# Kernel tuning notes

Hardware: AMD Instinct MI355X
Metric: run time of the kernel (lower is better)

## Reference

```python
import jax, jax.numpy as jnp
import numpy as np

N = 100000   # nodes
E = 1000000  # edges
IN, HID, OUT = 128, 64, 64


def setup_inputs() -> dict:
    key = jax.random.key(0)
    ks = jax.random.split(key, 6)
    x = jax.random.normal(ks[0], (N, IN), dtype=jnp.float32)
    edge_index = jax.random.randint(ks[1], (2, E), 0, N, dtype=jnp.int64)
    edge_attr = jax.random.uniform(ks[2], (E,), dtype=jnp.float32)
    # Glorot-style init like PyG GCNConv (weight [in, out], bias zeros)
    W1 = jax.random.normal(ks[3], (IN, HID), dtype=jnp.float32) * (1.0 / np.sqrt(IN))
    b1 = jnp.zeros((HID,), dtype=jnp.float32)
    W2 = jax.random.normal(ks[4], (HID, OUT), dtype=jnp.float32) * (1.0 / np.sqrt(HID))
    b2 = jnp.zeros((OUT,), dtype=jnp.float32)
    return {"x": x, "edge_index": edge_index, "edge_attr": edge_attr,
            "W1": W1, "b1": b1, "W2": W2, "b2": b2}


def gcn_conv(x, edge_index, edge_weight, W, b):
    """GCNConv: add self-loops, symmetric normalization, linear + scatter-add."""
    n = x.shape[0]
    row, col = edge_index[0], edge_index[1]
    loop = jnp.arange(n, dtype=row.dtype)
    row = jnp.concatenate([row, loop])
    col = jnp.concatenate([col, loop])
    w = jnp.concatenate([edge_weight, jnp.ones((n,), dtype=x.dtype)])
    deg = jax.ops.segment_sum(w, col, num_segments=n)              # [N]
    dinv = jnp.where(deg > 0, jax.lax.rsqrt(deg), 0.0)
    norm = dinv[row] * w * dinv[col]                               # [E+N]
    h = x @ W                                                      # [N, out]
    agg = jax.ops.segment_sum(h[row] * norm[:, None], col, num_segments=n)
    return agg + b


def reference(x, edge_index, edge_attr, W1, b1, W2, b2):
    h = jax.nn.relu(gcn_conv(x, edge_index, edge_attr, W1, b1))
    return jax.nn.relu(gcn_conv(h, edge_index, edge_attr, W2, b2))
```

## Files before the change

### kernel.cpp

```cpp
#include <hip/hip_runtime.h>


#define BNODES 128
#define LB 7
#define MAXBKT 1024
#define EPT 16
#define EPB (256 * EPT)

typedef __attribute__((ext_vector_type(8))) short bf16x8;
typedef __attribute__((ext_vector_type(4))) float f32x4;

__device__ __forceinline__ unsigned short f2bf(float f) {
    unsigned u = __float_as_uint(f);
    u = (u + 0x7FFF + ((u >> 16) & 1)) >> 16;
    return (unsigned short)u;
}
__device__ __forceinline__ float bf2f(unsigned short h) {
    return __uint_as_float(((unsigned)h) << 16);
}

__device__ __forceinline__ int waveIncScan(int v, int lane) {
    #pragma unroll
    for (int d = 1; d < 64; d <<= 1) {
        int u = __shfl_up(v, d, 64);
        if (lane >= d) v += u;
    }
    return v;
}

__device__ __forceinline__ int blockIncScan(int v, int t, int* wt) {
    int lane = t & 63, w = t >> 6;
    int s = waveIncScan(v, lane);
    if (lane == 63) wt[w] = s;
    __syncthreads();
    int add = 0;
    #pragma unroll
    for (int i = 0; i < 3; ++i) if (i < w) add += wt[i];
    return s + add;
}


__global__ __launch_bounds__(256) void hist_kernel(
    const int* __restrict__ col, int* __restrict__ H, int E, int NBKT,
    const float* __restrict__ W1, const float* __restrict__ W2,
    unsigned short* __restrict__ WT1, unsigned short* __restrict__ WT2, int NEB)
{
    int t = threadIdx.x, blk = blockIdx.x;
    if (blk >= NEB) {
        int i = (blk - NEB) * 256 + t;
        if (i < 64 * 128) {
            int c = i >> 7, k = i & 127;
            WT1[i] = f2bf(W1[k * 64 + c]);
        } else if (i < 64 * 128 + 64 * 64) {
            int j = i - 64 * 128;
            int c = j >> 6, k = j & 63;
            WT2[j] = f2bf(W2[k * 64 + c]);
        }
        return;
    }
    __shared__ int h[MAXBKT];
    for (int b = t; b < NBKT; b += 256) h[b] = 0;
    __syncthreads();
    int base = blk * EPB;
    #pragma unroll
    for (int i = 0; i < EPT; ++i) {
        int e = base + i * 256 + t;
        if (e < E) atomicAdd(&h[col[e] >> LB], 1);
    }
    __syncthreads();
    for (int b = t; b < NBKT; b += 256) H[blk * NBKT + b] = h[b];
}

__global__ __launch_bounds__(256) void rowscan_kernel(
    int* __restrict__ H, int* __restrict__ rowSum, int NEB, int NBKT)
{
    __shared__ int wt[4];
    int b = blockIdx.x, t = threadIdx.x;
    int v = (t < NEB) ? H[t * NBKT + b] : 0;
    int incl = blockIncScan(v, t, wt);
    if (t < NEB) H[t * NBKT + b] = incl - v;
    if (t == 255) rowSum[b] = incl;
}

__global__ __launch_bounds__(256) void bktscan_kernel(
    const int* __restrict__ rowSum, int* __restrict__ bktStart, int NBKT)
{
    __shared__ int wt[4];
    int t = threadIdx.x;
    int v[4]; int sum = 0;
    #pragma unroll
    for (int k = 0; k < 4; ++k) {
        int i = t * 4 + k;
        v[k] = (i < NBKT) ? rowSum[i] : 0;
        sum += v[k];
    }
    int incl = blockIncScan(sum, t, wt);
    int excl = incl - sum;
    #pragma unroll
    for (int k = 0; k < 4; ++k) {
        int i = t * 4 + k;
        if (i < NBKT) bktStart[i] = excl;
        excl += v[k];
    }
    if (t == 255) bktStart[NBKT] = incl;
}

__global__ __launch_bounds__(256) void scatter_kernel(
    const int* __restrict__ row, const int* __restrict__ col,
    const float* __restrict__ w, const int* __restrict__ H,
    const int* __restrict__ bktStart, int2* __restrict__ sedge1, int E, int NBKT)
{
    __shared__ int cur[MAXBKT];
    int t = threadIdx.x, blk = blockIdx.x;
    for (int b = t; b < NBKT; b += 256) cur[b] = bktStart[b] + H[blk * NBKT + b];
    __syncthreads();
    int base = blk * EPB;
    #pragma unroll
    for (int i = 0; i < EPT; ++i) {
        int e = base + i * 256 + t;
        if (e < E) {
            int c = col[e];
            int b = c >> LB;
            int pos = atomicAdd(&cur[b], 1);
            int2 pk;
            pk.x = row[e] | ((c & (BNODES - 1)) << 20);
            pk.y = __float_as_int(w[e]);
            sedge1[pos] = pk;
        }
    }
}

__global__ __launch_bounds__(256) void fine_kernel(
    const int2* __restrict__ sedge1, const int* __restrict__ bktStart,
    int2* __restrict__ sedge2, int* __restrict__ nodeStart,
    int* __restrict__ nodeCnt, float* __restrict__ dinv, int n)
{
    __shared__ int cnt[BNODES];
    __shared__ float wsum[BNODES];
    __shared__ int off[BNODES];
    __shared__ int cur[BNODES];
    __shared__ int wt[4];
    int b = blockIdx.x, t = threadIdx.x;
    if (t < BNODES) { cnt[t] = 0; wsum[t] = 1.0f; }
    __syncthreads();
    int s = bktStart[b], e = bktStart[b + 1];
    for (int j = s + t; j < e; j += 256) {
        int2 pk = sedge1[j];
        int ld = pk.x >> 20;
        atomicAdd(&cnt[ld], 1);
        atomicAdd(&wsum[ld], __int_as_float(pk.y));
    }
    __syncthreads();
    int v = (t < BNODES) ? cnt[t] : 0;
    int incl = blockIncScan(v, t, wt);
    if (t < BNODES) { off[t] = s + incl - v; cur[t] = s + incl - v; }
    __syncthreads();
    int node = b * BNODES + t;
    if (t < BNODES && node < n) {
        nodeStart[node] = off[t];
        nodeCnt[node] = cnt[t];
        dinv[node] = rsqrtf(wsum[t]);
    }
    for (int j = s + t; j < e; j += 256) {
        int2 pk = sedge1[j];
        int ld = pk.x >> 20;
        int pos = atomicAdd(&cur[ld], 1);
        sedge2[pos] = make_int2(pk.x & 0xFFFFF, pk.y);
    }
}

template<int K, bool IN_BF16>
__global__ __launch_bounds__(256) void gemm_mfma_kernel(
    const void* __restrict__ Xv, const unsigned short* __restrict__ WT,
    const float* __restrict__ dinv, unsigned short* __restrict__ G, int n)
{
    constexpr int ROWB = 2 * K;
    constexpr int SLOTS = K / 8;
    __shared__ char smem[64 * ROWB * 2];
    char* xs = smem;
    char* ws = smem + 64 * ROWB;
    const int tid = threadIdx.x;
    const int nodeBase = blockIdx.x * 64;

    for (int q = tid; q < 64 * SLOTS; q += 256) {
        int r = q / SLOTS, s = q % SLOTS;
        uint4 v = *(const uint4*)(WT + r * K + s * 8);
        *(uint4*)(ws + r * ROWB + ((s ^ (r & 7)) * 16)) = v;
    }
    constexpr int CPR = K / 4;
    if constexpr (IN_BF16) {
        const unsigned short* X = (const unsigned short*)Xv;
        for (int q = tid; q < 64 * CPR; q += 256) {
            int r = q / CPR, c = q % CPR;
            int node = nodeBase + r;
            uint2 v = make_uint2(0u, 0u);
            if (node < n) v = *(const uint2*)(X + (size_t)node * K + c * 4);
            *(uint2*)(xs + r * ROWB + (((c >> 1) ^ (r & 7)) * 16) + (c & 1) * 8) = v;
        }
    } else {
        const float* X = (const float*)Xv;
        for (int q = tid; q < 64 * CPR; q += 256) {
            int r = q / CPR, c = q % CPR;
            int node = nodeBase + r;
            float4 v = make_float4(0.f, 0.f, 0.f, 0.f);
            if (node < n) v = *(const float4*)(X + (size_t)node * K + c * 4);
            ushort4 h;
            h.x = f2bf(v.x); h.y = f2bf(v.y); h.z = f2bf(v.z); h.w = f2bf(v.w);
            *(ushort4*)(xs + r * ROWB + (((c >> 1) ^ (r & 7)) * 16) + (c & 1) * 8) = h;
        }
    }
    __syncthreads();

    const int lane = tid & 63;
    const int w = tid >> 6;
    const int lr = lane & 15;
    const int lk = lane >> 4;
    const int arow = (w << 4) + lr;

    f32x4 acc[4] = {};
    #pragma unroll
    for (int kb = 0; kb < K / 32; ++kb) {
        int s = kb * 4 + lk;
        bf16x8 a = *(bf16x8*)(xs + arow * ROWB + ((s ^ (arow & 7)) * 16));
        #pragma unroll
        for (int cb = 0; cb < 4; ++cb) {
            int c = cb * 16 + lr;
            bf16x8 b = *(bf16x8*)(ws + c * ROWB + ((s ^ (c & 7)) * 16));
            acc[cb] = __builtin_amdgcn_mfma_f32_16x16x32_bf16(a, b, acc[cb], 0, 0, 0);
        }
    }

    int rowbase = nodeBase + (w << 4) + (lk << 2);
    #pragma unroll
    for (int j = 0; j < 4; ++j) {
        int node = rowbase + j;
        if (node >= n) continue;
        float dv = dinv[node];
        #pragma unroll
        for (int cb = 0; cb < 4; ++cb)
            G[(size_t)node * 64 + cb * 16 + lr] = f2bf(acc[cb][j] * dv);
    }
}

__global__ __launch_bounds__(256) void aggmm_kernel(
    const unsigned short* __restrict__ G1, const int2* __restrict__ sedge2,
    const int* __restrict__ nodeStart, const int* __restrict__ nodeCnt,
    const float* __restrict__ dinv, const float* __restrict__ bias,
    const unsigned short* __restrict__ WT2, unsigned short* __restrict__ G2, int n)
{
    constexpr int ROWB = 128;
    __shared__ char smem[64 * ROWB * 2];
    char* xs = smem;
    char* ws = smem + 64 * ROWB;
    const int tid = threadIdx.x;
    const int nodeBase = blockIdx.x * 64;

    for (int q = tid; q < 64 * 8; q += 256) {
        int r = q >> 3, s = q & 7;
        uint4 v = *(const uint4*)(WT2 + r * 64 + s * 8);
        *(uint4*)(ws + r * ROWB + ((s ^ (r & 7)) * 16)) = v;
    }

    int p = tid & 15;
    float4 bb = *(const float4*)&bias[p * 4];
    #pragma unroll
    for (int pass = 0; pass < 4; ++pass) {
        int r = pass * 16 + (tid >> 4);
        int node = nodeBase + r;
        float4 o = make_float4(0.f, 0.f, 0.f, 0.f);
        if (node < n) {
            ushort4 sv = *(const ushort4*)&G1[(size_t)node * 64 + p * 4];
            float4 a0 = make_float4(bf2f(sv.x), bf2f(sv.y), bf2f(sv.z), bf2f(sv.w));
            float4 a1 = make_float4(0.f, 0.f, 0.f, 0.f);
            int s = nodeStart[node];
            int e_end = s + nodeCnt[node];
            int j = s;
            for (; j + 1 < e_end; j += 2) {
                int2 pk0 = sedge2[j];
                int2 pk1 = sedge2[j + 1];
                float w0 = __int_as_float(pk0.y);
                float w1 = __int_as_float(pk1.y);
                ushort4 g0 = *(const ushort4*)&G1[(size_t)pk0.x * 64 + p * 4];
                ushort4 g1 = *(const ushort4*)&G1[(size_t)pk1.x * 64 + p * 4];
                a0.x = fmaf(w0, bf2f(g0.x), a0.x); a0.y = fmaf(w0, bf2f(g0.y), a0.y);
                a0.z = fmaf(w0, bf2f(g0.z), a0.z); a0.w = fmaf(w0, bf2f(g0.w), a0.w);
                a1.x = fmaf(w1, bf2f(g1.x), a1.x); a1.y = fmaf(w1, bf2f(g1.y), a1.y);
                a1.z = fmaf(w1, bf2f(g1.z), a1.z); a1.w = fmaf(w1, bf2f(g1.w), a1.w);
            }
            if (j < e_end) {
                int2 pk = sedge2[j];
                float w = __int_as_float(pk.y);
                ushort4 g = *(const ushort4*)&G1[(size_t)pk.x * 64 + p * 4];
                a0.x = fmaf(w, bf2f(g.x), a0.x); a0.y = fmaf(w, bf2f(g.y), a0.y);
                a0.z = fmaf(w, bf2f(g.z), a0.z); a0.w = fmaf(w, bf2f(g.w), a0.w);
            }
            float di = dinv[node];
            o.x = fmaxf(fmaf(di, a0.x + a1.x, bb.x), 0.f);
            o.y = fmaxf(fmaf(di, a0.y + a1.y, bb.y), 0.f);
            o.z = fmaxf(fmaf(di, a0.z + a1.z, bb.z), 0.f);
            o.w = fmaxf(fmaf(di, a0.w + a1.w, bb.w), 0.f);
        }
        ushort4 h;
        h.x = f2bf(o.x); h.y = f2bf(o.y); h.z = f2bf(o.z); h.w = f2bf(o.w);
        *(ushort4*)(xs + r * ROWB + (((p >> 1) ^ (r & 7)) * 16) + (p & 1) * 8) = h;
    }
    __syncthreads();

    const int lane = tid & 63;
    const int w = tid >> 6;
    const int lr = lane & 15;
    const int lk = lane >> 4;
    const int arow = (w << 4) + lr;

    f32x4 acc[4] = {};
    #pragma unroll
    for (int kb = 0; kb < 2; ++kb) {
        int s = kb * 4 + lk;
        bf16x8 a = *(bf16x8*)(xs + arow * ROWB + ((s ^ (arow & 7)) * 16));
        #pragma unroll
        for (int cb = 0; cb < 4; ++cb) {
            int c = cb * 16 + lr;
            bf16x8 b = *(bf16x8*)(ws + c * ROWB + ((s ^ (c & 7)) * 16));
            acc[cb] = __builtin_amdgcn_mfma_f32_16x16x32_bf16(a, b, acc[cb], 0, 0, 0);
        }
    }

    int rowbase = nodeBase + (w << 4) + (lk << 2);
    #pragma unroll
    for (int j = 0; j < 4; ++j) {
        int node = rowbase + j;
        if (node >= n) continue;
        float dv = dinv[node];
        #pragma unroll
        for (int cb = 0; cb < 4; ++cb)
            G2[(size_t)node * 64 + cb * 16 + lr] = f2bf(acc[cb][j] * dv);
    }
}

__global__ __launch_bounds__(256) void agg_kernel(
    const unsigned short* __restrict__ G, const int2* __restrict__ sedge2,
    const int* __restrict__ nodeStart, const int* __restrict__ nodeCnt,
    const float* __restrict__ dinv, const float* __restrict__ bias,
    float* __restrict__ OUT, int n)
{
    int t = blockIdx.x * blockDim.x + threadIdx.x;
    if (t >= n * 16) return;
    int node = t >> 4, p = t & 15;

    ushort4 sv = *(const ushort4*)&G[(size_t)node * 64 + p * 4];
    float4 a0 = make_float4(bf2f(sv.x), bf2f(sv.y), bf2f(sv.z), bf2f(sv.w));
    float4 a1 = make_float4(0.f, 0.f, 0.f, 0.f);

    int s = nodeStart[node];
    int e_end = s + nodeCnt[node];
    int j = s;
    for (; j + 1 < e_end; j += 2) {
        int2 pk0 = sedge2[j];
        int2 pk1 = sedge2[j + 1];
        float w0 = __int_as_float(pk0.y);
        float w1 = __int_as_float(pk1.y);
        ushort4 g0 = *(const ushort4*)&G[(size_t)pk0.x * 64 + p * 4];
        ushort4 g1 = *(const ushort4*)&G[(size_t)pk1.x * 64 + p * 4];
        a0.x = fmaf(w0, bf2f(g0.x), a0.x); a0.y = fmaf(w0, bf2f(g0.y), a0.y);
        a0.z = fmaf(w0, bf2f(g0.z), a0.z); a0.w = fmaf(w0, bf2f(g0.w), a0.w);
        a1.x = fmaf(w1, bf2f(g1.x), a1.x); a1.y = fmaf(w1, bf2f(g1.y), a1.y);
        a1.z = fmaf(w1, bf2f(g1.z), a1.z); a1.w = fmaf(w1, bf2f(g1.w), a1.w);
    }
    if (j < e_end) {
        int2 pk = sedge2[j];
        float w = __int_as_float(pk.y);
        ushort4 g = *(const ushort4*)&G[(size_t)pk.x * 64 + p * 4];
        a0.x = fmaf(w, bf2f(g.x), a0.x); a0.y = fmaf(w, bf2f(g.y), a0.y);
        a0.z = fmaf(w, bf2f(g.z), a0.z); a0.w = fmaf(w, bf2f(g.w), a0.w);
    }

    float di = dinv[node];
    float4 bb = *(const float4*)&bias[p * 4];
    float4 o;
    o.x = fmaxf(fmaf(di, a0.x + a1.x, bb.x), 0.f);
    o.y = fmaxf(fmaf(di, a0.y + a1.y, bb.y), 0.f);
    o.z = fmaxf(fmaf(di, a0.z + a1.z, bb.z), 0.f);
    o.w = fmaxf(fmaf(di, a0.w + a1.w, bb.w), 0.f);
    *(float4*)&OUT[(size_t)node * 64 + p * 4] = o;
}

extern "C" void kernel_launch(void* const* d_in, const int* in_sizes, int n_in,
                              void* d_out, int out_size, void* d_ws, size_t ws_size,
                              hipStream_t stream) {
    const float* x     = (const float*)d_in[0];
    const int*   eidx  = (const int*)d_in[1];
    const float* eattr = (const float*)d_in[2];
    const float* W1    = (const float*)d_in[3];
    const float* b1    = (const float*)d_in[4];
    const float* W2    = (const float*)d_in[5];
    const float* b2    = (const float*)d_in[6];
    float* out = (float*)d_out;

    const int n = in_sizes[0] / 128;
    const int E = in_sizes[2];
    const int* row = eidx;
    const int* col = eidx + E;

    const int NBKT = (n + BNODES - 1) / BNODES;
    const int NEB  = (E + EPB - 1) / EPB;

    int2*  sedge1 = (int2*)d_ws;
    int2*  sedge2 = sedge1 + (size_t)E;
    unsigned short* g1 = (unsigned short*)(sedge2 + (size_t)E);
    unsigned short* g2 = g1 + (size_t)n * 64;
    unsigned short* WT1 = g2 + (size_t)n * 64;
    unsigned short* WT2 = WT1 + 64 * 128;
    float* dinv      = (float*)(WT2 + 64 * 64);
    int*   nodeStart = (int*)(dinv + n);
    int*   nodeCnt   = nodeStart + n;
    int*   H         = nodeCnt + n;
    int*   rowSum    = H + (size_t)NEB * NBKT;
    int*   bktStart  = rowSum + NBKT;

    const int nbG = (n + 63) / 64;
    const int nbA = (int)(((size_t)n * 16 + 255) / 256);

    hist_kernel<<<NEB + 48, 256, 0, stream>>>(col, H, E, NBKT, W1, W2, WT1, WT2, NEB);
    rowscan_kernel<<<NBKT, 256, 0, stream>>>(H, rowSum, NEB, NBKT);
    bktscan_kernel<<<1, 256, 0, stream>>>(rowSum, bktStart, NBKT);
    scatter_kernel<<<NEB, 256, 0, stream>>>(row, col, eattr, H, bktStart, sedge1, E, NBKT);
    fine_kernel<<<NBKT, 256, 0, stream>>>(sedge1, bktStart, sedge2, nodeStart, nodeCnt, dinv, n);

    gemm_mfma_kernel<128, false><<<nbG, 256, 0, stream>>>(x, WT1, dinv, g1, n);
    aggmm_kernel<<<nbG, 256, 0, stream>>>(g1, sedge2, nodeStart, nodeCnt, dinv, b1, WT2, g2, n);
    agg_kernel<<<nbA, 256, 0, stream>>>(g2, sedge2, nodeStart, nodeCnt, dinv, b2, out, n);
}
```

Measured before the change: 129.1 us.

## Merge edge scatter with first GEMM and apply dinv scaling in fine kernel

The first-layer GEMM no longer needs dinv, so it is launched as extra blocks of the scatter kernel and runs alongside the edge bucketing. The dinv row scaling of g1 moves into fine_kernel as a read-modify-write pass over each bucket's nodes. The gather loops are also unrolled by four with separate accumulators to give more memory-level parallelism. The trade-offs are an extra read and write of g1, a second bf16 rounding step, and a larger shared-memory footprint for the scatter blocks.

Measured after the change: 133.6 us. 3.5% more time.

```diff
diff --git a/kernel.cpp b/kernel.cpp
--- a/kernel.cpp
+++ b/kernel.cpp
@@ -105,121 +105,69 @@
     if (t == 255) bktStart[NBKT] = incl;
 }
 
-__global__ __launch_bounds__(256) void scatter_kernel(
+__global__ __launch_bounds__(256) void scatter_gemm_kernel(
     const int* __restrict__ row, const int* __restrict__ col,
     const float* __restrict__ w, const int* __restrict__ H,
-    const int* __restrict__ bktStart, int2* __restrict__ sedge1, int E, int NBKT)
-{
-    __shared__ int cur[MAXBKT];
-    int t = threadIdx.x, blk = blockIdx.x;
-    for (int b = t; b < NBKT; b += 256) cur[b] = bktStart[b] + H[blk * NBKT + b];
-    __syncthreads();
-    int base = blk * EPB;
-    #pragma unroll
-    for (int i = 0; i < EPT; ++i) {
-        int e = base + i * 256 + t;
-        if (e < E) {
-            int c = col[e];
-            int b = c >> LB;
-            int pos = atomicAdd(&cur[b], 1);
-            int2 pk;
-            pk.x = row[e] | ((c & (BNODES - 1)) << 20);
-            pk.y = __float_as_int(w[e]);
-            sedge1[pos] = pk;
+    const int* __restrict__ bktStart, int2* __restrict__ sedge1,
+    int E, int NBKT, int NEB,
+    const float* __restrict__ X, const unsigned short* __restrict__ WT,
+    unsigned short* __restrict__ G, int n)
+{
+    __shared__ char smem[64 * 256 * 2];
+    const int t = threadIdx.x;
+    const int blk = blockIdx.x;
+
+    if (blk < NEB) {
+        int* cur = (int*)smem;
+        for (int b = t; b < NBKT; b += 256) cur[b] = bktStart[b] + H[blk * NBKT + b];
+        __syncthreads();
+        int base = blk * EPB;
+        #pragma unroll
+        for (int i = 0; i < EPT; ++i) {
+            int e = base + i * 256 + t;
+            if (e < E) {
+                int c = col[e];
+                int b = c >> LB;
+                int pos = atomicAdd(&cur[b], 1);
+                int2 pk;
+                pk.x = row[e] | ((c & (BNODES - 1)) << 20);
+                pk.y = __float_as_int(w[e]);
+                sedge1[pos] = pk;
+            }
         }
-    }
-}
-
-__global__ __launch_bounds__(256) void fine_kernel(
-    const int2* __restrict__ sedge1, const int* __restrict__ bktStart,
-    int2* __restrict__ sedge2, int* __restrict__ nodeStart,
-    int* __restrict__ nodeCnt, float* __restrict__ dinv, int n)
-{
-    __shared__ int cnt[BNODES];
-    __shared__ float wsum[BNODES];
-    __shared__ int off[BNODES];
-    __shared__ int cur[BNODES];
-    __shared__ int wt[4];
-    int b = blockIdx.x, t = threadIdx.x;
-    if (t < BNODES) { cnt[t] = 0; wsum[t] = 1.0f; }
-    __syncthreads();
-    int s = bktStart[b], e = bktStart[b + 1];
-    for (int j = s + t; j < e; j += 256) {
-        int2 pk = sedge1[j];
-        int ld = pk.x >> 20;
-        atomicAdd(&cnt[ld], 1);
-        atomicAdd(&wsum[ld], __int_as_float(pk.y));
-    }
-    __syncthreads();
-    int v = (t < BNODES) ? cnt[t] : 0;
-    int incl = blockIncScan(v, t, wt);
-    if (t < BNODES) { off[t] = s + incl - v; cur[t] = s + incl - v; }
-    __syncthreads();
-    int node = b * BNODES + t;
-    if (t < BNODES && node < n) {
-        nodeStart[node] = off[t];
-        nodeCnt[node] = cnt[t];
-        dinv[node] = rsqrtf(wsum[t]);
-    }
-    for (int j = s + t; j < e; j += 256) {
-        int2 pk = sedge1[j];
-        int ld = pk.x >> 20;
-        int pos = atomicAdd(&cur[ld], 1);
-        sedge2[pos] = make_int2(pk.x & 0xFFFFF, pk.y);
-    }
-}
-
-template<int K, bool IN_BF16>
-__global__ __launch_bounds__(256) void gemm_mfma_kernel(
-    const void* __restrict__ Xv, const unsigned short* __restrict__ WT,
-    const float* __restrict__ dinv, unsigned short* __restrict__ G, int n)
-{
-    constexpr int ROWB = 2 * K;
-    constexpr int SLOTS = K / 8;
-    __shared__ char smem[64 * ROWB * 2];
+        return;
+    }
+
+    constexpr int K = 128, ROWB = 256, SLOTS = 16, CPR = 32;
     char* xs = smem;
     char* ws = smem + 64 * ROWB;
-    const int tid = threadIdx.x;
-    const int nodeBase = blockIdx.x * 64;
-
-    for (int q = tid; q < 64 * SLOTS; q += 256) {
+    const int nodeBase = (blk - NEB) * 64;
+
+    for (int q = t; q < 64 * SLOTS; q += 256) {
         int r = q / SLOTS, s = q % SLOTS;
         uint4 v = *(const uint4*)(WT + r * K + s * 8);
         *(uint4*)(ws + r * ROWB + ((s ^ (r & 7)) * 16)) = v;
     }
-    constexpr int CPR = K / 4;
-    if constexpr (IN_BF16) {
-        const unsigned short* X = (const unsigned short*)Xv;
-        for (int q = tid; q < 64 * CPR; q += 256) {
-            int r = q / CPR, c = q % CPR;
-            int node = nodeBase + r;
-            uint2 v = make_uint2(0u, 0u);
-            if (node < n) v = *(const uint2*)(X + (size_t)node * K + c * 4);
-            *(uint2*)(xs + r * ROWB + (((c >> 1) ^ (r & 7)) * 16) + (c & 1) * 8) = v;
-        }
-    } else {
-        const float* X = (const float*)Xv;
-        for (int q = tid; q < 64 * CPR; q += 256) {
-            int r = q / CPR, c = q % CPR;
-            int node = nodeBase + r;
-            float4 v = make_float4(0.f, 0.f, 0.f, 0.f);
-            if (node < n) v = *(const float4*)(X + (size_t)node * K + c * 4);
-            ushort4 h;
-            h.x = f2bf(v.x); h.y = f2bf(v.y); h.z = f2bf(v.z); h.w = f2bf(v.w);
-            *(ushort4*)(xs + r * ROWB + (((c >> 1) ^ (r & 7)) * 16) + (c & 1) * 8) = h;
-        }
-    }
-    __syncthreads();
-
-    const int lane = tid & 63;
-    const int w = tid >> 6;
+    for (int q = t; q < 64 * CPR; q += 256) {
+        int r = q / CPR, c = q % CPR;
+        int node = nodeBase + r;
+        float4 v = make_float4(0.f, 0.f, 0.f, 0.f);
+        if (node < n) v = *(const float4*)(X + (size_t)node * K + c * 4);
+        ushort4 h;
+        h.x = f2bf(v.x); h.y = f2bf(v.y); h.z = f2bf(v.z); h.w = f2bf(v.w);
+        *(ushort4*)(xs + r * ROWB + (((c >> 1) ^ (r & 7)) * 16) + (c & 1) * 8) = h;
+    }
+    __syncthreads();
+
+    const int lane = t & 63;
+    const int wv = t >> 6;
     const int lr = lane & 15;
     const int lk = lane >> 4;
-    const int arow = (w << 4) + lr;
+    const int arow = (wv << 4) + lr;
 
     f32x4 acc[4] = {};
     #pragma unroll
-    for (int kb = 0; kb < K / 32; ++kb) {
+    for (int kb = 0; kb < 4; ++kb) {
         int s = kb * 4 + lk;
         bf16x8 a = *(bf16x8*)(xs + arow * ROWB + ((s ^ (arow & 7)) * 16));
         #pragma unroll
@@ -230,16 +178,114 @@
         }
     }
 
-    int rowbase = nodeBase + (w << 4) + (lk << 2);
+    int rowbase = nodeBase + (wv << 4) + (lk << 2);
     #pragma unroll
     for (int j = 0; j < 4; ++j) {
         int node = rowbase + j;
         if (node >= n) continue;
-        float dv = dinv[node];
         #pragma unroll
         for (int cb = 0; cb < 4; ++cb)
-            G[(size_t)node * 64 + cb * 16 + lr] = f2bf(acc[cb][j] * dv);
-    }
+            G[(size_t)node * 64 + cb * 16 + lr] = f2bf(acc[cb][j]);
+    }
+}
+
+__global__ __launch_bounds__(256) void fine_kernel(
+    const int2* __restrict__ sedge1, const int* __restrict__ bktStart,
+    int2* __restrict__ sedge2, int* __restrict__ nodeStart,
+    int* __restrict__ nodeCnt, float* __restrict__ dinv,
+    unsigned short* __restrict__ g1, int n)
+{
+    __shared__ int cnt[BNODES];
+    __shared__ float wsum[BNODES];
+    __shared__ int off[BNODES];
+    __shared__ int cur[BNODES];
+    __shared__ float dloc[BNODES];
+    __shared__ int wt[4];
+    int b = blockIdx.x, t = threadIdx.x;
+    if (t < BNODES) { cnt[t] = 0; wsum[t] = 1.0f; }
+    __syncthreads();
+    int s = bktStart[b], e = bktStart[b + 1];
+    for (int j = s + t; j < e; j += 256) {
+        int2 pk = sedge1[j];
+        int ld = pk.x >> 20;
+        atomicAdd(&cnt[ld], 1);
+        atomicAdd(&wsum[ld], __int_as_float(pk.y));
+    }
+    __syncthreads();
+    int v = (t < BNODES) ? cnt[t] : 0;
+    int incl = blockIncScan(v, t, wt);
+    if (t < BNODES) {
+        off[t] = s + incl - v;
+        cur[t] = s + incl - v;
+        dloc[t] = rsqrtf(wsum[t]);
+    }
+    __syncthreads();
+    int node = b * BNODES + t;
+    if (t < BNODES && node < n) {
+        nodeStart[node] = off[t];
+        nodeCnt[node] = cnt[t];
+        dinv[node] = dloc[t];
+    }
+    for (int j = s + t; j < e; j += 256) {
+        int2 pk = sedge1[j];
+        int ld = pk.x >> 20;
+        int pos = atomicAdd(&cur[ld], 1);
+        sedge2[pos] = make_int2(pk.x & 0xFFFFF, pk.y);
+    }
+    for (int q = t; q < BNODES * 8; q += 256) {
+        int r = q >> 3, cc = q & 7;
+        int nd = b * BNODES + r;
+        if (nd >= n) continue;
+        float dv = dloc[r];
+        size_t offb = (size_t)nd * 64 + cc * 8;
+        ushort4 u0 = *(const ushort4*)(g1 + offb);
+        ushort4 u1 = *(const ushort4*)(g1 + offb + 4);
+        u0.x = f2bf(bf2f(u0.x) * dv); u0.y = f2bf(bf2f(u0.y) * dv);
+        u0.z = f2bf(bf2f(u0.z) * dv); u0.w = f2bf(bf2f(u0.w) * dv);
+        u1.x = f2bf(bf2f(u1.x) * dv); u1.y = f2bf(bf2f(u1.y) * dv);
+        u1.z = f2bf(bf2f(u1.z) * dv); u1.w = f2bf(bf2f(u1.w) * dv);
+        *(ushort4*)(g1 + offb) = u0;
+        *(ushort4*)(g1 + offb + 4) = u1;
+    }
+}
+
+__device__ __forceinline__ float4 gather_accum(
+    const unsigned short* __restrict__ G, const int2* __restrict__ eb,
+    int m, int p, float4 a0)
+{
+    float4 a1 = make_float4(0.f, 0.f, 0.f, 0.f);
+    float4 a2 = make_float4(0.f, 0.f, 0.f, 0.f);
+    float4 a3 = make_float4(0.f, 0.f, 0.f, 0.f);
+    int j = 0;
+    for (; j + 3 < m; j += 4) {
+        int2 pk0 = eb[j], pk1 = eb[j + 1], pk2 = eb[j + 2], pk3 = eb[j + 3];
+        ushort4 g0 = *(const ushort4*)&G[(size_t)pk0.x * 64 + p * 4];
+        ushort4 g1 = *(const ushort4*)&G[(size_t)pk1.x * 64 + p * 4];
+        ushort4 g2 = *(const ushort4*)&G[(size_t)pk2.x * 64 + p * 4];
+        ushort4 g3 = *(const ushort4*)&G[(size_t)pk3.x * 64 + p * 4];
+        float w0 = __int_as_float(pk0.y), w1 = __int_as_float(pk1.y);
+        float w2 = __int_as_float(pk2.y), w3 = __int_as_float(pk3.y);
+        a0.x = fmaf(w0, bf2f(g0.x), a0.x); a0.y = fmaf(w0, bf2f(g0.y), a0.y);
+        a0.z = fmaf(w0, bf2f(g0.z), a0.z); a0.w = fmaf(w0, bf2f(g0.w), a0.w);
+        a1.x = fmaf(w1, bf2f(g1.x), a1.x); a1.y = fmaf(w1, bf2f(g1.y), a1.y);
+        a1.z = fmaf(w1, bf2f(g1.z), a1.z); a1.w = fmaf(w1, bf2f(g1.w), a1.w);
+        a2.x = fmaf(w2, bf2f(g2.x), a2.x); a2.y = fmaf(w2, bf2f(g2.y), a2.y);
+        a2.z = fmaf(w2, bf2f(g2.z), a2.z); a2.w = fmaf(w2, bf2f(g2.w), a2.w);
+        a3.x = fmaf(w3, bf2f(g3.x), a3.x); a3.y = fmaf(w3, bf2f(g3.y), a3.y);
+        a3.z = fmaf(w3, bf2f(g3.z), a3.z); a3.w = fmaf(w3, bf2f(g3.w), a3.w);
+    }
+    for (; j < m; ++j) {
+        int2 pk = eb[j];
+        float w = __int_as_float(pk.y);
+        ushort4 g = *(const ushort4*)&G[(size_t)pk.x * 64 + p * 4];
+        a0.x = fmaf(w, bf2f(g.x), a0.x); a0.y = fmaf(w, bf2f(g.y), a0.y);
+        a0.z = fmaf(w, bf2f(g.z), a0.z); a0.w = fmaf(w, bf2f(g.w), a0.w);
+    }
+    a0.x += a1.x + a2.x + a3.x;
+    a0.y += a1.y + a2.y + a3.y;
+    a0.z += a1.z + a2.z + a3.z;
+    a0.w += a1.w + a2.w + a3.w;
+    return a0;
 }
 
 __global__ __launch_bounds__(256) void aggmm_kernel(
@@ -270,35 +316,14 @@
         float4 o = make_float4(0.f, 0.f, 0.f, 0.f);
         if (node < n) {
             ushort4 sv = *(const ushort4*)&G1[(size_t)node * 64 + p * 4];
-            float4 a0 = make_float4(bf2f(sv.x), bf2f(sv.y), bf2f(sv.z), bf2f(sv.w));
-            float4 a1 = make_float4(0.f, 0.f, 0.f, 0.f);
+            float4 a = make_float4(bf2f(sv.x), bf2f(sv.y), bf2f(sv.z), bf2f(sv.w));
             int s = nodeStart[node];
-            int e_end = s + nodeCnt[node];
-            int j = s;
-            for (; j + 1 < e_end; j += 2) {
-                int2 pk0 = sedge2[j];
-                int2 pk1 = sedge2[j + 1];
-                float w0 = __int_as_float(pk0.y);
-                float w1 = __int_as_float(pk1.y);
-                ushort4 g0 = *(const ushort4*)&G1[(size_t)pk0.x * 64 + p * 4];
-                ushort4 g1 = *(const ushort4*)&G1[(size_t)pk1.x * 64 + p * 4];
-                a0.x = fmaf(w0, bf2f(g0.x), a0.x); a0.y = fmaf(w0, bf2f(g0.y), a0.y);
-                a0.z = fmaf(w0, bf2f(g0.z), a0.z); a0.w = fmaf(w0, bf2f(g0.w), a0.w);
-                a1.x = fmaf(w1, bf2f(g1.x), a1.x); a1.y = fmaf(w1, bf2f(g1.y), a1.y);
-                a1.z = fmaf(w1, bf2f(g1.z), a1.z); a1.w = fmaf(w1, bf2f(g1.w), a1.w);
-            }
-            if (j < e_end) {
-                int2 pk = sedge2[j];
-                float w = __int_as_float(pk.y);
-                ushort4 g = *(const ushort4*)&G1[(size_t)pk.x * 64 + p * 4];
-                a0.x = fmaf(w, bf2f(g.x), a0.x); a0.y = fmaf(w, bf2f(g.y), a0.y);
-                a0.z = fmaf(w, bf2f(g.z), a0.z); a0.w = fmaf(w, bf2f(g.w), a0.w);
-            }
+            a = gather_accum(G1, sedge2 + s, nodeCnt[node], p, a);
             float di = dinv[node];
-            o.x = fmaxf(fmaf(di, a0.x + a1.x, bb.x), 0.f);
-            o.y = fmaxf(fmaf(di, a0.y + a1.y, bb.y), 0.f);
-            o.z = fmaxf(fmaf(di, a0.z + a1.z, bb.z), 0.f);
-            o.w = fmaxf(fmaf(di, a0.w + a1.w, bb.w), 0.f);
+            o.x = fmaxf(fmaf(di, a.x, bb.x), 0.f);
+            o.y = fmaxf(fmaf(di, a.y, bb.y), 0.f);
+            o.z = fmaxf(fmaf(di, a.z, bb.z), 0.f);
+            o.w = fmaxf(fmaf(di, a.w, bb.w), 0.f);
         }
         ushort4 h;
         h.x = f2bf(o.x); h.y = f2bf(o.y); h.z = f2bf(o.z); h.w = f2bf(o.w);
@@ -348,39 +373,17 @@
     int node = t >> 4, p = t & 15;
 
     ushort4 sv = *(const ushort4*)&G[(size_t)node * 64 + p * 4];
-    float4 a0 = make_float4(bf2f(sv.x), bf2f(sv.y), bf2f(sv.z), bf2f(sv.w));
-    float4 a1 = make_float4(0.f, 0.f, 0.f, 0.f);
-
+    float4 a = make_float4(bf2f(sv.x), bf2f(sv.y), bf2f(sv.z), bf2f(sv.w));
     int s = nodeStart[node];
-    int e_end = s + nodeCnt[node];
-    int j = s;
-    for (; j + 1 < e_end; j += 2) {
-        int2 pk0 = sedge2[j];
-        int2 pk1 = sedge2[j + 1];
-        float w0 = __int_as_float(pk0.y);
-        float w1 = __int_as_float(pk1.y);
-        ushort4 g0 = *(const ushort4*)&G[(size_t)pk0.x * 64 + p * 4];
-        ushort4 g1 = *(const ushort4*)&G[(size_t)pk1.x * 64 + p * 4];
-        a0.x = fmaf(w0, bf2f(g0.x), a0.x); a0.y = fmaf(w0, bf2f(g0.y), a0.y);
-        a0.z = fmaf(w0, bf2f(g0.z), a0.z); a0.w = fmaf(w0, bf2f(g0.w), a0.w);
-        a1.x = fmaf(w1, bf2f(g1.x), a1.x); a1.y = fmaf(w1, bf2f(g1.y), a1.y);
-        a1.z = fmaf(w1, bf2f(g1.z), a1.z); a1.w = fmaf(w1, bf2f(g1.w), a1.w);
-    }
-    if (j < e_end) {
-        int2 pk = sedge2[j];
-        float w = __int_as_float(pk.y);
-        ushort4 g = *(const ushort4*)&G[(size_t)pk.x * 64 + p * 4];
-        a0.x = fmaf(w, bf2f(g.x), a0.x); a0.y = fmaf(w, bf2f(g.y), a0.y);
-        a0.z = fmaf(w, bf2f(g.z), a0.z); a0.w = fmaf(w, bf2f(g.w), a0.w);
-    }
+    a = gather_accum(G, sedge2 + s, nodeCnt[node], p, a);
 
     float di = dinv[node];
     float4 bb = *(const float4*)&bias[p * 4];
     float4 o;
-    o.x = fmaxf(fmaf(di, a0.x + a1.x, bb.x), 0.f);
-    o.y = fmaxf(fmaf(di, a0.y + a1.y, bb.y), 0.f);
-    o.z = fmaxf(fmaf(di, a0.z + a1.z, bb.z), 0.f);
-    o.w = fmaxf(fmaf(di, a0.w + a1.w, bb.w), 0.f);
+    o.x = fmaxf(fmaf(di, a.x, bb.x), 0.f);
+    o.y = fmaxf(fmaf(di, a.y, bb.y), 0.f);
+    o.z = fmaxf(fmaf(di, a.z, bb.z), 0.f);
+    o.w = fmaxf(fmaf(di, a.w, bb.w), 0.f);
     *(float4*)&OUT[(size_t)node * 64 + p * 4] = o;
 }
 
@@ -423,10 +426,11 @@
     hist_kernel<<<NEB + 48, 256, 0, stream>>>(col, H, E, NBKT, W1, W2, WT1, WT2, NEB);
     rowscan_kernel<<<NBKT, 256, 0, stream>>>(H, rowSum, NEB, NBKT);
     bktscan_kernel<<<1, 256, 0, stream>>>(rowSum, bktStart, NBKT);
-    scatter_kernel<<<NEB, 256, 0, stream>>>(row, col, eattr, H, bktStart, sedge1, E, NBKT);
-    fine_kernel<<<NBKT, 256, 0, stream>>>(sedge1, bktStart, sedge2, nodeStart, nodeCnt, dinv, n);
-
-    gemm_mfma_kernel<128, false><<<nbG, 256, 0, stream>>>(x, WT1, dinv, g1, n);
+    scatter_gemm_kernel<<<NEB + nbG, 256, 0, stream>>>(
+        row, col, eattr, H, bktStart, sedge1, E, NBKT, NEB, x, WT1, g1, n);
+    fine_kernel<<<NBKT, 256, 0, stream>>>(sedge1, bktStart, sedge2, nodeStart,
+                                          nodeCnt, dinv, g1, n);
+
     aggmm_kernel<<<nbG, 256, 0, stream>>>(g1, sedge2, nodeStart, nodeCnt, dinv, b1, WT2, g2, n);
     agg_kernel<<<nbA, 256, 0, stream>>>(g2, sedge2, nodeStart, nodeCnt, dinv, b2, out, n);
 }
```
